# Performance work log

Measured on AMD Instinct MI355X. Metric: run time of the kernel, lower is better.

## Reference

```python
import jax, jax.numpy as jnp
import numpy as np

B, T, C, U = 256, 512, 256, 64  # batch, time, classes (incl. blank), label length
BLANK = C - 1                   # keras ctc_batch_cost: blank is last class
S = 2 * U + 1                   # extended label length (blanks interleaved)
NEG = -1e30                     # safe log-zero for fp32
EPS = 1e-7                      # keras.backend.epsilon()


def setup_inputs() -> dict:
    key = jax.random.key(0)
    k1, k2 = jax.random.split(key)
    # y_pred are softmax probabilities over time, as fed to ctc_batch_cost
    y_pred = jax.nn.softmax(jax.random.normal(k1, (B, T, C), dtype=jnp.float32), axis=-1)
    # labels exclude the blank index (values in [0, C-2]); all U positions valid
    y_true = jax.random.randint(k2, (B, U), 0, C - 1, dtype=jnp.int32)
    return {"y_true": y_true, "y_pred": y_pred}


def _ctc_loss(y_pred, y_true):
    # keras ctc_batch_cost computes loss on log(y_pred + eps)
    log_probs = jnp.log(y_pred + EPS)                      # [B, T, C]
    # extended label sequence: blank, l1, blank, l2, ..., blank
    ext = jnp.full((B, S), BLANK, dtype=y_true.dtype).at[:, 1::2].set(y_true)
    # gather per-state emission log-probs: lp_ext[b,t,s] = log_probs[b,t,ext[b,s]]
    lp_ext = jnp.take_along_axis(log_probs, ext[:, None, :].astype(jnp.int32), axis=2)  # [B,T,S]
    # skip transition (s-2 -> s) allowed iff ext[s] != blank and ext[s] != ext[s-2]
    ext_m2 = jnp.pad(ext[:, :-2], ((0, 0), (2, 0)), constant_values=-1)
    skip_ok = (ext != BLANK) & (ext != ext_m2)             # [B, S]

    # alpha_0: can start in state 0 (blank) or state 1 (first label)
    alpha0 = (jnp.full((B, S), NEG, dtype=jnp.float32)
              .at[:, 0].set(lp_ext[:, 0, 0])
              .at[:, 1].set(lp_ext[:, 0, 1]))

    def step(alpha, lp_t):
        a1 = jnp.pad(alpha[:, :-1], ((0, 0), (1, 0)), constant_values=NEG)
        a2 = jnp.pad(alpha[:, :-2], ((0, 0), (2, 0)), constant_values=NEG)
        a2 = jnp.where(skip_ok, a2, NEG)
        alpha = jnp.logaddexp(jnp.logaddexp(alpha, a1), a2) + lp_t
        return alpha, None

    lp_time_major = jnp.swapaxes(lp_ext, 0, 1)             # [T, B, S]
    alpha, _ = jax.lax.scan(step, alpha0, lp_time_major[1:])
    # terminate in last blank or last label
    loss = -jnp.logaddexp(alpha[:, -1], alpha[:, -2])      # [B]
    return loss[:, None]                                   # [B, 1] like ctc_batch_cost


def reference(y_true, y_pred):
    return _ctc_loss(y_pred, y_true)
```

## Files before the change

### kernel.cpp

```cpp
#include <hip/hip_runtime.h>


constexpr int B = 256, T = 512, C = 256, U = 64;
constexpr int CH = 16;
constexpr int NBUF = 4;
#define EPSF 1e-7f

__device__ __forceinline__ float dpp_wave_shr1(float x) {
    return __int_as_float(__builtin_amdgcn_update_dpp(
        0, __float_as_int(x), 0x138, 0xf, 0xf, true));
}

#define DPPMAX(ctrl)                                                      \
    {                                                                     \
        float x_ = __int_as_float(__builtin_amdgcn_update_dpp(            \
            0, __float_as_int(m_), (ctrl), 0xf, 0xf, true));              \
        m_ = fmaxf(m_, x_);                                               \
    }

#define RESCALE()                                                         \
    {                                                                     \
        float m_ = fmaxf(fmaxf(a_even, a_odd), a_top);                    \
        DPPMAX(0x111) DPPMAX(0x112) DPPMAX(0x114) DPPMAX(0x118)           \
        DPPMAX(0x142) DPPMAX(0x143)                                       \
        const float mx_ = __int_as_float(                                 \
            __builtin_amdgcn_readlane(__float_as_int(m_), 63));           \
        int e_ = (__float_as_int(mx_) >> 23) & 0xff;                      \
        int k_ = 187 - e_;                                                \
        k_ = k_ > 127 ? 127 : k_;                                         \
        const float s_ = __int_as_float((k_ + 127) << 23);                \
        a_even *= s_; a_odd *= s_; a_top *= s_;                           \
        esum += k_;                                                       \
    }

#define STAGE(cc)                                                          \
    {                                                                      \
        const int cs_ = (cc);                                              \
        float* lbase_ = &rows[cs_ % NBUF][0][0];                           \
        _Pragma("unroll")                                                  \
        for (int i = 0; i < CH; ++i) {                                     \
            int t = 1 + cs_ * CH + i;                                      \
            t = t < T ? t : T - 1;                                         \
            const float* g_ = rowp + (size_t)t * C + (lane << 2);          \
            __builtin_amdgcn_global_load_lds(                              \
                (const __attribute__((address_space(1))) void*)g_,         \
                (__attribute__((address_space(3))) void*)(lbase_ + i * C), \
                16, 0, 0);                                                 \
        }                                                                  \
    }

#define LDS_READ_ASM(cc)                                                   \
    {                                                                      \
        const int cr_ = (cc);                                              \
        float(*row_)[C] = rows[cr_ % NBUF];                                \
        const unsigned labA_ = (unsigned)(size_t)                          \
            (__attribute__((address_space(3))) void*)&row_[0][label];      \
        const unsigned blkA_ = (unsigned)(size_t)                          \
            (__attribute__((address_space(3))) void*)&row_[0][C - 1];      \
        _Pragma("unroll")                                                  \
        for (int i = 0; i < CH; ++i) {                                     \
            asm volatile("ds_read_b32 %0, %1"                              \
                         : "=v"(lab[i]) : "v"(labA_ + i * 1024));          \
            asm volatile("ds_read_b32 %0, %1"                              \
                         : "=v"(blk[i]) : "v"(blkA_ + i * 1024));          \
        }                                                                  \
        asm volatile("s_waitcnt lgkmcnt(0)" ::: "memory");                 \
        __builtin_amdgcn_sched_barrier(0);                                 \
    }

#define COMP_CHUNK(NSTEPS)                                                 \
    {                                                                      \
        _Pragma("unroll")                                                  \
        for (int i = 0; i < (NSTEPS); ++i) {                               \
            const float pb = blk[i] + EPSF;                                \
            const float pl = lab[i] + EPSF;                                \
            const float po = dpp_wave_shr1(a_odd);                         \
            const float skp = skip_ok ? po : 0.f;                          \
            const float ne = (a_even + po) * pb;                           \
            const float no = (a_odd + a_even + skp) * pl;                  \
            const float nt = (a_top + a_odd) * pb;                         \
            a_even = ne; a_odd = no; a_top = nt;                           \
            if (((1 + i) & 7) == 0) RESCALE();                             \
        }                                                                  \
    }

__global__ __launch_bounds__(64) void ctc_kernel(const int* __restrict__ y_true,
                                                 const float* __restrict__ y_pred,
                                                 float* __restrict__ out) {
    __shared__ float rows[NBUF][CH][C];
    const int b = blockIdx.x;
    const int lane = threadIdx.x;
    const int label = y_true[b * U + lane];
    const int label_prev = __shfl_up(label, 1);
    const bool skip_ok = (lane > 0) && (label != label_prev);
    const float* __restrict__ rowp = y_pred + (size_t)b * (T * C);

    float a_even, a_odd, a_top;
    {
        const float pb = rowp[C - 1] + EPSF;
        const float pl = rowp[label] + EPSF;
        a_even = (lane == 0) ? pb : 0.f;
        a_odd  = (lane == 0) ? pl : 0.f;
        a_top  = 0.f;
    }
    int esum = 0;

    STAGE(0);
    STAGE(1);
    STAGE(2);

    float lab[CH], blk[CH];

    for (int c = 0; c < 30; ++c) {
        asm volatile("s_waitcnt vmcnt(32)" ::: "memory");
        __builtin_amdgcn_sched_barrier(0);
        if (c <= 28) STAGE(c + 3);
        LDS_READ_ASM(c);
        COMP_CHUNK(CH);
    }

    {
        asm volatile("s_waitcnt vmcnt(16)" ::: "memory");
        __builtin_amdgcn_sched_barrier(0);
        LDS_READ_ASM(30);
        COMP_CHUNK(CH);
    }
    {
        asm volatile("s_waitcnt vmcnt(0)" ::: "memory");
        __builtin_amdgcn_sched_barrier(0);
        LDS_READ_ASM(31);
        COMP_CHUNK(CH - 1);
    }

    if (lane == 63)
        out[b] = -logf(a_top + a_odd) + (float)esum * 0.69314718055994531f;
}

extern "C" void kernel_launch(void* const* d_in, const int* in_sizes, int n_in,
                              void* d_out, int out_size, void* d_ws, size_t ws_size,
                              hipStream_t stream) {
    const int* y_true   = (const int*)d_in[0];
    const float* y_pred = (const float*)d_in[1];
    float* out = (float*)d_out;
    hipLaunchKernelGGL(ctc_kernel, dim3(B), dim3(64), 0, stream,
                       y_true, y_pred, out);
}
```

Before: 194.5 us.

## Split CTC kernel into producer and consumer wavefronts with packed LDS handoff

Adds a second wavefront per block that issues the global-to-LDS loads and gathers each lane's label and blank probabilities into a packed double-buffered LDS array. The compute wavefront then reads one 64-bit value per timestep instead of two scattered 32-bit reads, and no longer waits on global memory itself. This aims to take load latency and gather work off the serial recurrence critical path, at the cost of a block barrier per chunk and double the threads per block.

```diff
diff --git a/kernel.cpp b/kernel.cpp
--- a/kernel.cpp
+++ b/kernel.cpp
@@ -5,6 +5,8 @@
 constexpr int CH = 16;
 constexpr int NBUF = 4;
 #define EPSF 1e-7f
+
+typedef float f2 __attribute__((ext_vector_type(2)));
 
 __device__ __forceinline__ float dpp_wave_shr1(float x) {
     return __int_as_float(__builtin_amdgcn_update_dpp(
@@ -49,21 +51,66 @@
         }                                                                  \
     }
 
-#define LDS_READ_ASM(cc)                                                   \
-    {                                                                      \
-        const int cr_ = (cc);                                              \
-        float(*row_)[C] = rows[cr_ % NBUF];                                \
+#define DSR(dst, addr, OS)                                                 \
+    asm volatile("ds_read_b32 %0, %1 offset:" OS                           \
+                 : "=v"(dst) : "v"(addr));
+
+#define DSR64(dst, addr, OS)                                               \
+    asm volatile("ds_read_b64 %0, %1 offset:" OS                           \
+                 : "=v"(dst) : "v"(addr));
+
+#define PACK(cc)                                                           \
+    {                                                                      \
+        const int cp_ = (cc);                                              \
+        float(*row_)[C] = rows[cp_ % NBUF];                                \
         const unsigned labA_ = (unsigned)(size_t)                          \
             (__attribute__((address_space(3))) void*)&row_[0][label];      \
         const unsigned blkA_ = (unsigned)(size_t)                          \
             (__attribute__((address_space(3))) void*)&row_[0][C - 1];      \
+        DSR(lv[0],  labA_, "0")     DSR(lv[1],  labA_, "1024")             \
+        DSR(lv[2],  labA_, "2048")  DSR(lv[3],  labA_, "3072")             \
+        DSR(lv[4],  labA_, "4096")  DSR(lv[5],  labA_, "5120")             \
+        DSR(lv[6],  labA_, "6144")  DSR(lv[7],  labA_, "7168")             \
+        DSR(lv[8],  labA_, "8192")  DSR(lv[9],  labA_, "9216")             \
+        DSR(lv[10], labA_, "10240") DSR(lv[11], labA_, "11264")            \
+        DSR(lv[12], labA_, "12288") DSR(lv[13], labA_, "13312")            \
+        DSR(lv[14], labA_, "14336") DSR(lv[15], labA_, "15360")            \
+        DSR(bv[0],  blkA_, "0")     DSR(bv[1],  blkA_, "1024")             \
+        DSR(bv[2],  blkA_, "2048")  DSR(bv[3],  blkA_, "3072")             \
+        DSR(bv[4],  blkA_, "4096")  DSR(bv[5],  blkA_, "5120")             \
+        DSR(bv[6],  blkA_, "6144")  DSR(bv[7],  blkA_, "7168")             \
+        DSR(bv[8],  blkA_, "8192")  DSR(bv[9],  blkA_, "9216")             \
+        DSR(bv[10], blkA_, "10240") DSR(bv[11], blkA_, "11264")            \
+        DSR(bv[12], blkA_, "12288") DSR(bv[13], blkA_, "13312")            \
+        DSR(bv[14], blkA_, "14336") DSR(bv[15], blkA_, "15360")            \
+        asm volatile("s_waitcnt lgkmcnt(0)" ::: "memory");                 \
+        __builtin_amdgcn_sched_barrier(0);                                 \
+        f2* dst_ = &pk[cp_ & 1][0][lane];                                  \
         _Pragma("unroll")                                                  \
         for (int i = 0; i < CH; ++i) {                                     \
-            asm volatile("ds_read_b32 %0, %1"                              \
-                         : "=v"(lab[i]) : "v"(labA_ + i * 1024));          \
-            asm volatile("ds_read_b32 %0, %1"                              \
-                         : "=v"(blk[i]) : "v"(blkA_ + i * 1024));          \
+            f2 t_; t_.x = lv[i]; t_.y = bv[i];                             \
+            dst_[i * 64] = t_;                                             \
         }                                                                  \
+    }
+
+#define FLUSHBAR()                                                         \
+    asm volatile("s_waitcnt lgkmcnt(0)" ::: "memory");                     \
+    __builtin_amdgcn_sched_barrier(0);                                     \
+    __builtin_amdgcn_s_barrier();
+
+#define READPK(cc)                                                         \
+    {                                                                      \
+        const unsigned pA_ = (unsigned)(size_t)                            \
+            (__attribute__((address_space(3))) void*)                      \
+            &pk[(cc) & 1][0][lane];                                        \
+        DSR64(lb[0],  pA_, "0")    DSR64(lb[1],  pA_, "512")               \
+        DSR64(lb[2],  pA_, "1024") DSR64(lb[3],  pA_, "1536")              \
+        DSR64(lb[4],  pA_, "2048") DSR64(lb[5],  pA_, "2560")              \
+        DSR64(lb[6],  pA_, "3072") DSR64(lb[7],  pA_, "3584")              \
+        DSR64(lb[8],  pA_, "4096") DSR64(lb[9],  pA_, "4608")              \
+        DSR64(lb[10], pA_, "5120") DSR64(lb[11], pA_, "5632")              \
+        DSR64(lb[12], pA_, "6144") DSR64(lb[13], pA_, "6656")              \
+        DSR64(lb[14], pA_, "7168") DSR64(lb[15], pA_, "7680")              \
         asm volatile("s_waitcnt lgkmcnt(0)" ::: "memory");                 \
         __builtin_amdgcn_sched_barrier(0);                                 \
     }
@@ -72,8 +119,8 @@
     {                                                                      \
         _Pragma("unroll")                                                  \
         for (int i = 0; i < (NSTEPS); ++i) {                               \
-            const float pb = blk[i] + EPSF;                                \
-            const float pl = lab[i] + EPSF;                                \
+            const float pb = lb[i].y + EPSF;                               \
+            const float pl = lb[i].x + EPSF;                               \
             const float po = dpp_wave_shr1(a_odd);                         \
             const float skp = skip_ok ? po : 0.f;                          \
             const float ne = (a_even + po) * pb;                           \
@@ -84,56 +131,67 @@
         }                                                                  \
     }
 
-__global__ __launch_bounds__(64) void ctc_kernel(const int* __restrict__ y_true,
-                                                 const float* __restrict__ y_pred,
-                                                 float* __restrict__ out) {
+__global__ __launch_bounds__(128) void ctc_kernel(const int* __restrict__ y_true,
+                                                  const float* __restrict__ y_pred,
+                                                  float* __restrict__ out) {
     __shared__ float rows[NBUF][CH][C];
+    __shared__ f2 pk[2][CH][64];
     const int b = blockIdx.x;
-    const int lane = threadIdx.x;
+    const int tid = threadIdx.x;
+    const int lane = tid & 63;
+    const int wid = tid >> 6;
     const int label = y_true[b * U + lane];
-    const int label_prev = __shfl_up(label, 1);
-    const bool skip_ok = (lane > 0) && (label != label_prev);
     const float* __restrict__ rowp = y_pred + (size_t)b * (T * C);
 
-    float a_even, a_odd, a_top;
-    {
-        const float pb = rowp[C - 1] + EPSF;
-        const float pl = rowp[label] + EPSF;
-        a_even = (lane == 0) ? pb : 0.f;
-        a_odd  = (lane == 0) ? pl : 0.f;
-        a_top  = 0.f;
-    }
-    int esum = 0;
-
-    STAGE(0);
-    STAGE(1);
-    STAGE(2);
-
-    float lab[CH], blk[CH];
-
-    for (int c = 0; c < 30; ++c) {
-        asm volatile("s_waitcnt vmcnt(32)" ::: "memory");
-        __builtin_amdgcn_sched_barrier(0);
-        if (c <= 28) STAGE(c + 3);
-        LDS_READ_ASM(c);
-        COMP_CHUNK(CH);
-    }
-
-    {
+    if (wid == 1) {
+        float lv[CH], bv[CH];
+        STAGE(0);
+        STAGE(1);
+        STAGE(2);
+        for (int c = 0; c < 30; ++c) {
+            asm volatile("s_waitcnt vmcnt(32)" ::: "memory");
+            __builtin_amdgcn_sched_barrier(0);
+            PACK(c);
+            if (c <= 28) STAGE(c + 3);
+            FLUSHBAR();
+        }
         asm volatile("s_waitcnt vmcnt(16)" ::: "memory");
         __builtin_amdgcn_sched_barrier(0);
-        LDS_READ_ASM(30);
-        COMP_CHUNK(CH);
-    }
-    {
+        PACK(30);
+        FLUSHBAR();
         asm volatile("s_waitcnt vmcnt(0)" ::: "memory");
         __builtin_amdgcn_sched_barrier(0);
-        LDS_READ_ASM(31);
+        PACK(31);
+        FLUSHBAR();
+        __builtin_amdgcn_s_barrier();
+    } else {
+        const int label_prev = __shfl_up(label, 1);
+        const bool skip_ok = (lane > 0) && (label != label_prev);
+
+        float a_even, a_odd, a_top;
+        {
+            const float pb = rowp[C - 1] + EPSF;
+            const float pl = rowp[label] + EPSF;
+            a_even = (lane == 0) ? pb : 0.f;
+            a_odd  = (lane == 0) ? pl : 0.f;
+            a_top  = 0.f;
+        }
+        int esum = 0;
+
+        f2 lb[CH];
+        __builtin_amdgcn_s_barrier();
+        for (int cc = 0; cc < 31; ++cc) {
+            READPK(cc);
+            COMP_CHUNK(CH);
+            __builtin_amdgcn_s_barrier();
+        }
+        READPK(31);
         COMP_CHUNK(CH - 1);
-    }
-
-    if (lane == 63)
-        out[b] = -logf(a_top + a_odd) + (float)esum * 0.69314718055994531f;
+        __builtin_amdgcn_s_barrier();
+
+        if (lane == 63)
+            out[b] = -logf(a_top + a_odd) + (float)esum * 0.69314718055994531f;
+    }
 }
 
 extern "C" void kernel_launch(void* const* d_in, const int* in_sizes, int n_in,
@@ -142,6 +200,6 @@
     const int* y_true   = (const int*)d_in[0];
     const float* y_pred = (const float*)d_in[1];
     float* out = (float*)d_out;
-    hipLaunchKernelGGL(ctc_kernel, dim3(B), dim3(64), 0, stream,
+    hipLaunchKernelGGL(ctc_kernel, dim3(B), dim3(128), 0, stream,
                        y_true, y_pred, out);
 }
```

After: 193.8 us. Within noise of the previous version (-0.3%).
